# Kernel tuning notes

Measured on AMD Instinct MI355X. Metric: run time of the kernel, lower is better.

Reference implementation:

```python
import jax, jax.numpy as jnp
import numpy as np

N = 50000      # nodes
E = 800000     # edges (before self-loops)
D = 128        # hid_d
H = 8          # heads
C = D // H     # per-head channels
L = 3          # layers
SLOPE = 0.2    # GATv2 leaky_relu negative slope
EPS = 1e-5     # LayerNorm eps


def setup_inputs() -> dict:
    key = jax.random.key(0)
    ks = jax.random.split(key, 8)
    x = jax.random.normal(ks[0], (N, D), dtype=jnp.float32)
    ei = jax.random.randint(ks[1], (2, E), 0, N, dtype=jnp.int32)
    s = 1.0 / np.sqrt(D)
    Wl = jax.random.normal(ks[2], (L, D, D), dtype=jnp.float32) * s   # source transform per layer
    Wr = jax.random.normal(ks[3], (L, D, D), dtype=jnp.float32) * s   # target transform per layer
    att = jax.random.normal(ks[4], (L, H, C), dtype=jnp.float32) * (1.0 / np.sqrt(C))
    bias = jnp.zeros((L, D), dtype=jnp.float32)
    gamma = jnp.ones((L, D), dtype=jnp.float32)
    beta = jnp.zeros((L, D), dtype=jnp.float32)
    return {"x": x, "Wl": Wl, "Wr": Wr, "att": att, "bias": bias,
            "gamma": gamma, "beta": beta, "ei": ei}


def _layernorm(y, g, b):
    mu = jnp.mean(y, axis=-1, keepdims=True)
    var = jnp.mean(jnp.square(y - mu), axis=-1, keepdims=True)
    return (y - mu) * jax.lax.rsqrt(var + EPS) * g + b


def reference(x, Wl, Wr, att, bias, gamma, beta, ei):
    # append self-loops (PyG GATv2Conv default add_self_loops=True)
    loops = jnp.arange(N, dtype=ei.dtype)
    src = jnp.concatenate([ei[0], loops])  # [E+N]
    dst = jnp.concatenate([ei[1], loops])  # [E+N]
    h = x
    for l in range(L):
        xl = (h @ Wl[l]).reshape(N, H, C)   # source-side features
        xr = (h @ Wr[l]).reshape(N, H, C)   # target-side features
        feat = xl[src] + xr[dst]            # [E+N, H, C] per-edge gather
        logits = jnp.einsum('ehc,hc->eh', jax.nn.leaky_relu(feat, SLOPE), att[l])
        # segment softmax over incoming edges of each dst node
        m = jax.ops.segment_max(logits, dst, num_segments=N)
        ex = jnp.exp(logits - m[dst])
        denom = jax.ops.segment_sum(ex, dst, num_segments=N)
        alpha = ex / denom[dst]             # [E+N, H]
        msg = alpha[:, :, None] * xl[src]   # [E+N, H, C]
        out = jax.ops.segment_sum(msg, dst, num_segments=N).reshape(N, H * C) + bias[l]
        # wrapper: h = h + dropout(elu(norm(gat(h)))) ; dropout = identity (eval)
        h = h + jax.nn.elu(_layernorm(out, gamma[l], beta[l]))
    return h
```

## Files before the change

### kernel.cpp

```cpp
#include <hip/hip_runtime.h>
#include <hip/hip_fp16.h>
#include <math.h>

#define N_NODES 50000
#define N_EDGES 800000
#define D 128
#define L 3
#define SLOPE 0.2f
#define LN_EPS 1e-5f
#define ETOT (N_EDGES + N_NODES)
#define SCAN_BLOCKS ((N_NODES + 1023) / 1024)

typedef _Float16 half8 __attribute__((ext_vector_type(8)));
typedef _Float16 h4v  __attribute__((ext_vector_type(4)));
typedef _Float16 h2v  __attribute__((ext_vector_type(2)));
typedef float f32x4 __attribute__((ext_vector_type(4)));


__global__ void rank_hist_kernel(const int* __restrict__ ei, int* __restrict__ counts,
                                 int* __restrict__ rank) {
    int idx = blockIdx.x * blockDim.x + threadIdx.x;
    if (idx >= ETOT) return;
    int d = (idx < N_EDGES) ? ei[N_EDGES + idx] : (idx - N_EDGES);
    rank[idx] = atomicAdd(&counts[d], 1);
}

__global__ __launch_bounds__(1024) void scan1_kernel(const int* __restrict__ counts,
                                                     int* __restrict__ offsets,
                                                     int* __restrict__ bsum,
                                                     int* __restrict__ blockhist) {
    __shared__ int wsum[16];
    __shared__ int lh[256];
    int tid = threadIdx.x;
    if (tid < 256) lh[tid] = 0;
    __syncthreads();
    int lane = tid & 63, w = tid >> 6;
    int i = blockIdx.x * 1024 + tid;
    int v = (i < N_NODES) ? counts[i] : 0;
    if (i < N_NODES) {
        int d = v; if (d > 255) d = 255;
        atomicAdd(&lh[d], 1);
    }
    int sc = v;
    #pragma unroll
    for (int off = 1; off < 64; off <<= 1) {
        int u = __shfl_up(sc, off);
        if (lane >= off) sc += u;
    }
    if (lane == 63) wsum[w] = sc;
    __syncthreads();
    if (w == 0) {
        int t2 = (lane < 16) ? wsum[lane] : 0;
        #pragma unroll
        for (int off = 1; off < 16; off <<= 1) {
            int u = __shfl_up(t2, off);
            if (lane >= off) t2 += u;
        }
        if (lane < 16) wsum[lane] = t2;
    }
    __syncthreads();
    int wpref = (w == 0) ? 0 : wsum[w - 1];
    if (i < N_NODES) offsets[i] = wpref + sc - v;
    if (tid == 0) bsum[blockIdx.x] = wsum[15];
    __syncthreads();
    if (tid < 256) blockhist[blockIdx.x * 256 + tid] = lh[tid];
}

__global__ __launch_bounds__(256) void scan2_kernel(const int* __restrict__ bsum,
                                                    int* __restrict__ bpre,
                                                    int* __restrict__ blockhist) {
    int tid = threadIdx.x;
    if (tid < 64) {
        int lane = tid;
        int v = (lane < SCAN_BLOCKS) ? bsum[lane] : 0;
        int sc = v;
        #pragma unroll
        for (int off = 1; off < 64; off <<= 1) {
            int u = __shfl_up(sc, off);
            if (lane >= off) sc += u;
        }
        if (lane < SCAN_BLOCKS) bpre[lane] = sc - v;
    }
    int d = tid;
    int run = 0;
    #pragma unroll 1
    for (int b = 0; b < SCAN_BLOCKS; ++b) {
        int c = blockhist[b * 256 + d];
        blockhist[b * 256 + d] = run;
        run += c;
    }
    __shared__ int wsum[4];
    int lane = d & 63, w = d >> 6;
    int sc = run;
    #pragma unroll
    for (int off = 1; off < 64; off <<= 1) {
        int u = __shfl_up(sc, off);
        if (lane >= off) sc += u;
    }
    if (lane == 63) wsum[w] = sc;
    __syncthreads();
    int wpre = 0;
    #pragma unroll
    for (int k = 0; k < 4; ++k) wpre += (k < w) ? wsum[k] : 0;
    int binbase = wpre + sc - run;
    #pragma unroll 1
    for (int b = 0; b < SCAN_BLOCKS; ++b)
        blockhist[b * 256 + d] += binbase;
}

__global__ __launch_bounds__(1024) void scan3_kernel(int* __restrict__ offsets,
                                                     const int* __restrict__ bpre,
                                                     const int* __restrict__ counts,
                                                     const int* __restrict__ blockhist,
                                                     int* __restrict__ perm) {
    __shared__ int lh[256];
    int tid = threadIdx.x;
    if (tid < 256) lh[tid] = 0;
    __syncthreads();
    int i = blockIdx.x * 1024 + tid;
    if (i < N_NODES) {
        offsets[i] += bpre[blockIdx.x];
        int d = counts[i]; if (d > 255) d = 255;
        int r = atomicAdd(&lh[d], 1);
        perm[blockhist[blockIdx.x * 256 + d] + r] = i;
    }
    if (i == 0) offsets[N_NODES] = ETOT;
}

__global__ void scatter_kernel(const int* __restrict__ ei, const int* __restrict__ offsets,
                               const int* __restrict__ rank,
                               unsigned short* __restrict__ sorted16) {
    int idx = blockIdx.x * blockDim.x + threadIdx.x;
    if (idx >= ETOT) return;
    int s, d;
    if (idx < N_EDGES) { s = ei[idx]; d = ei[N_EDGES + idx]; }
    else               { s = d = idx - N_EDGES; }
    sorted16[offsets[d] + rank[idx]] = (unsigned short)s;
}


__global__ __launch_bounds__(256) void wfrag_kernel(const float* __restrict__ Wl,
                                                    const float* __restrict__ Wr,
                                                    _Float16* __restrict__ Wfrag) {
    int u = blockIdx.x * 256 + threadIdx.x;
    if (u >= 3 * 4096) return;
    int lane = u & 63, nt = (u >> 6) & 7, kt = (u >> 9) & 3, y = (u >> 11) & 1, l = u >> 12;
    int r = lane & 15, q = lane >> 4;
    const float* W = (y ? Wr : Wl) + (size_t)l * D * D;
    half8 v;
    #pragma unroll
    for (int j = 0; j < 8; ++j)
        v[j] = (_Float16)W[(kt * 32 + q * 8 + j) * D + nt * 16 + r];
    *(half8*)&Wfrag[(size_t)u * 8] = v;
}


template<bool AHALF>
__global__ __launch_bounds__(256) void gemm_mfma_kernel(
        const void* __restrict__ hsrc, const _Float16* __restrict__ WfragL,
        _Float16* __restrict__ xlh, _Float16* __restrict__ xrh) {
    __shared__ half8 Afrag[1024];
    int t = threadIdx.x;
    int row0 = blockIdx.x * 64;
    int w = t >> 6, lane = t & 63;
    int y = w >> 1, nh = w & 1;

    half8 bfrag[16];
    #pragma unroll
    for (int kt = 0; kt < 4; ++kt)
        #pragma unroll
        for (int f = 0; f < 4; ++f) {
            int nt = nh * 4 + f;
            bfrag[kt * 4 + f] =
                *(const half8*)&WfragL[(size_t)(((y * 4 + kt) * 8 + nt) * 64 + lane) * 8];
        }

    {
        int kt = t >> 6, q = (t >> 4) & 3, r = t & 15;
        int kc = kt * 4 + q;
        #pragma unroll
        for (int i = 0; i < 4; ++i) {
            int row = row0 + i * 16 + r;
            half8 v = {};
            if (row < N_NODES) {
                if constexpr (AHALF) {
                    const _Float16* h16 = (const _Float16*)hsrc;
                    v = *(const half8*)&h16[(size_t)row * D + kc * 8];
                } else {
                    const float* p = &((const float*)hsrc)[(size_t)row * D + kc * 8];
                    float4 f0 = *(const float4*)p;
                    float4 f1 = *(const float4*)(p + 4);
                    v[0] = (_Float16)f0.x; v[1] = (_Float16)f0.y;
                    v[2] = (_Float16)f0.z; v[3] = (_Float16)f0.w;
                    v[4] = (_Float16)f1.x; v[5] = (_Float16)f1.y;
                    v[6] = (_Float16)f1.z; v[7] = (_Float16)f1.w;
                }
            }
            Afrag[i * 256 + t] = v;
        }
    }
    __syncthreads();

    f32x4 acc[16];
    #pragma unroll
    for (int i = 0; i < 16; ++i) acc[i] = (f32x4){0.f, 0.f, 0.f, 0.f};
    #pragma unroll
    for (int ntile = 0; ntile < 4; ++ntile) {
        #pragma unroll
        for (int kt = 0; kt < 4; ++kt) {
            half8 a = Afrag[ntile * 256 + kt * 64 + lane];
            #pragma unroll
            for (int f = 0; f < 4; ++f)
                acc[f * 4 + ntile] = __builtin_amdgcn_mfma_f32_16x16x32_f16(
                    bfrag[kt * 4 + f], a, acc[f * 4 + ntile], 0, 0, 0);
        }
    }

    _Float16* out = y ? xrh : xlh;
    int nr = lane & 15, fq = lane >> 4;
    #pragma unroll
    for (int ntile = 0; ntile < 4; ++ntile) {
        int row = row0 + ntile * 16 + nr;
        if (row < N_NODES) {
            #pragma unroll
            for (int f = 0; f < 4; ++f) {
                int fb = nh * 64 + f * 16 + fq * 4;
                h4v v4;
                v4[0] = (_Float16)acc[f * 4 + ntile][0];
                v4[1] = (_Float16)acc[f * 4 + ntile][1];
                v4[2] = (_Float16)acc[f * 4 + ntile][2];
                v4[3] = (_Float16)acc[f * 4 + ntile][3];
                *(h4v*)&out[(size_t)row * D + fb] = v4;
            }
        }
    }
}


__device__ __forceinline__ float pair_reduce2(float p) {
    int t;
    t = __builtin_amdgcn_update_dpp(0, __float_as_int(p), 0xB1, 0xF, 0xF, true);
    p += __int_as_float(t);
    return p;
}

__device__ __forceinline__ float logit8(half8 v, half8 xr, const h2v* att4, h2v slope2) {
    float p = 0.f;
    #pragma unroll
    for (int i = 0; i < 4; ++i) {
        h2v a; a[0] = v[2 * i];  a[1] = v[2 * i + 1];
        h2v b; b[0] = xr[2 * i]; b[1] = xr[2 * i + 1];
        h2v f  = a + b;
        h2v lf = __builtin_elementwise_max(f, f * slope2);
        p = __builtin_amdgcn_fdot2(lf, att4[i], p, false);
    }
    return p;
}

template<int KUN, bool MASK>
__device__ __forceinline__ void edge_block(
        int j, int idx_bp, unsigned off, unsigned laneoff, const char* xlb,
        half8 xr8, const h2v* att4, h2v slope2, int cnt,
        float& s, float* acc) {
    half8 vs[KUN];
    #pragma unroll
    for (int k = 0; k < KUN; ++k) {
        int o = __builtin_amdgcn_ds_bpermute(idx_bp + 4 * (j + k), (int)off);
        vs[k] = *(const half8*)(xlb + ((unsigned)o + laneoff));
    }
    #pragma unroll
    for (int k = 0; k < KUN; ++k) {
        float p = logit8(vs[k], xr8, att4, slope2);
        p = pair_reduce2(p);
        float e = __builtin_amdgcn_exp2f(p);
        if (MASK) e = (j + k < cnt) ? e : 0.f;
        s += e;
        #pragma unroll
        for (int i = 0; i < 8; ++i)
            acc[i] = fmaf(e, (float)vs[k][i], acc[i]);
    }
}

__global__ __launch_bounds__(256) void gat_node_kernel(
        const _Float16* __restrict__ xlh, const _Float16* __restrict__ xrh,
        const int* __restrict__ offsets, const unsigned short* __restrict__ sorted16,
        const int* __restrict__ perm,
        const float* __restrict__ att_l, const float* __restrict__ bias_l,
        const float* __restrict__ gamma_l, const float* __restrict__ beta_l,
        const float* __restrict__ hin, float* __restrict__ hout,
        _Float16* __restrict__ h16out) {
    int wid = (blockIdx.x * blockDim.x + threadIdx.x) >> 6;
    if (wid * 4 >= N_NODES) return;
    int lane = threadIdx.x & 63;
    int g = lane >> 4, hl = lane & 15;
    int node = perm[N_NODES - 4 - wid * 4 + g];
    unsigned laneoff = hl * 16u;
    int idx_bp = g << 6;

    half8 xr8 = *(const half8*)&xrh[(size_t)node * D + hl * 8];
    float4 af0 = *(const float4*)&att_l[hl * 8];
    float4 af1 = *(const float4*)&att_l[hl * 8 + 4];
    h2v att4[4], slope2;
    att4[0][0] = (_Float16)(af0.x * 1.44269504f);
    att4[0][1] = (_Float16)(af0.y * 1.44269504f);
    att4[1][0] = (_Float16)(af0.z * 1.44269504f);
    att4[1][1] = (_Float16)(af0.w * 1.44269504f);
    att4[2][0] = (_Float16)(af1.x * 1.44269504f);
    att4[2][1] = (_Float16)(af1.y * 1.44269504f);
    att4[3][0] = (_Float16)(af1.z * 1.44269504f);
    att4[3][1] = (_Float16)(af1.w * 1.44269504f);
    slope2[0] = (_Float16)SLOPE;
    slope2[1] = (_Float16)SLOPE;

    int beg = offsets[node], end = offsets[node + 1];
    int deg = end - beg;
    int d0 = __builtin_amdgcn_readlane(deg, 0);
    int d1 = __builtin_amdgcn_readlane(deg, 16);
    int d2 = __builtin_amdgcn_readlane(deg, 32);
    int d3 = __builtin_amdgcn_readlane(deg, 48);
    int m01 = d0 > d1 ? d0 : d1, m23 = d2 > d3 ? d2 : d3;
    int degMax = m01 > m23 ? m01 : m23;
    int n01 = d0 < d1 ? d0 : d1, n23 = d2 < d3 ? d2 : d3;
    int degMin = n01 < n23 ? n01 : n23;

    float s = 0.f;
    float acc[8] = {0.f, 0.f, 0.f, 0.f, 0.f, 0.f, 0.f, 0.f};
    const char* xlb = (const char*)xlh;

    for (int c0 = 0; c0 < degMax; c0 += 16) {
        int rem = deg - c0;
        int cnt = rem > 16 ? 16 : rem;
        int cl  = cnt > 0 ? (hl < cnt ? hl : cnt - 1) : 0;
        int pos = cnt > 0 ? beg + c0 + cl : beg;
        unsigned off = ((unsigned)sorted16[pos]) << 8;
        int jmax = degMax - c0; if (jmax > 16) jmax = 16;
        int nfull = degMin - c0; if (nfull > 16) nfull = 16; if (nfull < 0) nfull = 0;
        int j = 0;
        for (; j + 8 <= nfull; j += 8)
            edge_block<8, false>(j, idx_bp, off, laneoff, xlb, xr8, att4, slope2,
                                 cnt, s, acc);
        for (; j + 4 <= nfull; j += 4)
            edge_block<4, false>(j, idx_bp, off, laneoff, xlb, xr8, att4, slope2,
                                 cnt, s, acc);
        for (; j + 4 <= jmax; j += 4)
            edge_block<4, true>(j, idx_bp, off, laneoff, xlb, xr8, att4, slope2,
                                cnt, s, acc);
        for (; j < jmax; ++j)
            edge_block<1, true>(j, idx_bp, off, laneoff, xlb, xr8, att4, slope2,
                                cnt, s, acc);
    }

    float inv = 1.f / s;
    float4 b0 = *(const float4*)&bias_l[hl * 8];
    float4 b1 = *(const float4*)&bias_l[hl * 8 + 4];
    float o[8];
    o[0] = acc[0] * inv + b0.x; o[1] = acc[1] * inv + b0.y;
    o[2] = acc[2] * inv + b0.z; o[3] = acc[3] * inv + b0.w;
    o[4] = acc[4] * inv + b1.x; o[5] = acc[5] * inv + b1.y;
    o[6] = acc[6] * inv + b1.z; o[7] = acc[7] * inv + b1.w;
    float sum = ((o[0] + o[1]) + (o[2] + o[3])) + ((o[4] + o[5]) + (o[6] + o[7]));
    float sq  = ((o[0] * o[0] + o[1] * o[1]) + (o[2] * o[2] + o[3] * o[3]))
              + ((o[4] * o[4] + o[5] * o[5]) + (o[6] * o[6] + o[7] * o[7]));
    #pragma unroll
    for (int msk = 1; msk < 16; msk <<= 1) {
        sum += __shfl_xor(sum, msk);
        sq  += __shfl_xor(sq, msk);
    }
    float mu   = sum * (1.f / 128.f);
    float var  = sq * (1.f / 128.f) - mu * mu;
    float rstd = rsqrtf(var + LN_EPS);
    float4 g0 = *(const float4*)&gamma_l[hl * 8];
    float4 g1 = *(const float4*)&gamma_l[hl * 8 + 4];
    float4 e0 = *(const float4*)&beta_l[hl * 8];
    float4 e1 = *(const float4*)&beta_l[hl * 8 + 4];
    float gam[8] = {g0.x, g0.y, g0.z, g0.w, g1.x, g1.y, g1.z, g1.w};
    float bet[8] = {e0.x, e0.y, e0.z, e0.w, e1.x, e1.y, e1.z, e1.w};
    size_t di = (size_t)node * D + hl * 8;
    float4 h0 = *(const float4*)&hin[di];
    float4 h1 = *(const float4*)&hin[di + 4];
    float hv[8] = {h0.x, h0.y, h0.z, h0.w, h1.x, h1.y, h1.z, h1.w};
    float y[8];
    #pragma unroll
    for (int i = 0; i < 8; ++i) {
        float t = (o[i] - mu) * rstd * gam[i] + bet[i];
        t = t > 0.f ? t : __expf(t) - 1.f;
        y[i] = hv[i] + t;
    }
    float4 w0 = make_float4(y[0], y[1], y[2], y[3]);
    float4 w1 = make_float4(y[4], y[5], y[6], y[7]);
    *(float4*)&hout[di]     = w0;
    *(float4*)&hout[di + 4] = w1;
    half8 h16v;
    #pragma unroll
    for (int i = 0; i < 8; ++i) h16v[i] = (_Float16)y[i];
    *(half8*)&h16out[di] = h16v;
}


extern "C" void kernel_launch(void* const* d_in, const int* in_sizes, int n_in,
                              void* d_out, int out_size, void* d_ws, size_t ws_size,
                              hipStream_t stream) {
    const float* x     = (const float*)d_in[0];
    const float* Wl    = (const float*)d_in[1];
    const float* Wr    = (const float*)d_in[2];
    const float* att   = (const float*)d_in[3];
    const float* bias  = (const float*)d_in[4];
    const float* gamma = (const float*)d_in[5];
    const float* beta  = (const float*)d_in[6];
    const int*   ei    = (const int*)d_in[7];
    float* h = (float*)d_out;

    char* ws = (char*)d_ws;
    _Float16* xlh = (_Float16*)ws;   ws += (size_t)N_NODES * D * sizeof(_Float16);
    _Float16* xrh = (_Float16*)ws;   ws += (size_t)N_NODES * D * sizeof(_Float16);
    _Float16* h16 = (_Float16*)ws;   ws += (size_t)N_NODES * D * sizeof(_Float16);
    _Float16* Wfrag = (_Float16*)ws; ws += (size_t)3 * 4096 * 8 * sizeof(_Float16);
    int* offsets = (int*)ws;         ws += (size_t)(N_NODES + 4) * sizeof(int);
    int* counts  = (int*)ws;         ws += (size_t)N_NODES * sizeof(int);
    int* bsum    = (int*)ws;         ws += 64 * sizeof(int);
    int* bpre    = (int*)ws;         ws += 64 * sizeof(int);
    int* blockhist = (int*)ws;       ws += (size_t)SCAN_BLOCKS * 256 * sizeof(int);
    int* perm    = (int*)ws;         ws += (size_t)N_NODES * sizeof(int);
    int* rank    = (int*)ws;         ws += (size_t)ETOT * sizeof(int);
    unsigned short* sorted16 = (unsigned short*)ws;

    wfrag_kernel<<<48, 256, 0, stream>>>(Wl, Wr, Wfrag);
    (void)hipMemsetAsync(counts, 0, (size_t)N_NODES * sizeof(int), stream);
    rank_hist_kernel<<<(ETOT + 255) / 256, 256, 0, stream>>>(ei, counts, rank);
    scan1_kernel<<<SCAN_BLOCKS, 1024, 0, stream>>>(counts, offsets, bsum, blockhist);
    scan2_kernel<<<1, 256, 0, stream>>>(bsum, bpre, blockhist);
    scan3_kernel<<<SCAN_BLOCKS, 1024, 0, stream>>>(offsets, bpre, counts, blockhist, perm);
    scatter_kernel<<<(ETOT + 255) / 256, 256, 0, stream>>>(ei, offsets, rank, sorted16);

    int gat_waves  = (N_NODES + 3) / 4;
    int gat_blocks = (gat_waves * 64 + 255) / 256;
    for (int l = 0; l < L; ++l) {
        const float* hin = (l == 0) ? x : h;
        if (l == 0)
            gemm_mfma_kernel<false><<<(N_NODES + 63) / 64, 256, 0, stream>>>(
                x, Wfrag + (size_t)l * 4096 * 8, xlh, xrh);
        else
            gemm_mfma_kernel<true><<<(N_NODES + 63) / 64, 256, 0, stream>>>(
                h16, Wfrag + (size_t)l * 4096 * 8, xlh, xrh);
        gat_node_kernel<<<gat_blocks, 256, 0, stream>>>(
            xlh, xrh, offsets, sorted16, perm,
            att + (size_t)l * D, bias + (size_t)l * D,
            gamma + (size_t)l * D, beta + (size_t)l * D, hin, h, h16);
    }
}
```

Baseline: 327.4 us.

## Fuse per-layer GEMM and GAT aggregation into one cooperative persistent kernel

Merges the MFMA projection kernel and the per-node attention/aggregation kernel into a single cooperative kernel per layer. A grid-wide sync separates the two phases, and each phase uses grid-stride loops over tiles and node groups. Grid size comes from an occupancy query that is cached in statics. This removes a kernel launch and its tail per layer, but register pressure from the GEMM phase may reduce occupancy for the latency-bound gather phase.

```diff
diff --git a/kernel.cpp b/kernel.cpp
--- a/kernel.cpp
+++ b/kernel.cpp
@@ -1,6 +1,9 @@
 #include <hip/hip_runtime.h>
+#include <hip/hip_cooperative_groups.h>
 #include <hip/hip_fp16.h>
 #include <math.h>
+
+namespace cg = cooperative_groups;
 
 #define N_NODES 50000
 #define N_EDGES 800000
@@ -155,88 +158,6 @@
 }
 
 
-template<bool AHALF>
-__global__ __launch_bounds__(256) void gemm_mfma_kernel(
-        const void* __restrict__ hsrc, const _Float16* __restrict__ WfragL,
-        _Float16* __restrict__ xlh, _Float16* __restrict__ xrh) {
-    __shared__ half8 Afrag[1024];
-    int t = threadIdx.x;
-    int row0 = blockIdx.x * 64;
-    int w = t >> 6, lane = t & 63;
-    int y = w >> 1, nh = w & 1;
-
-    half8 bfrag[16];
-    #pragma unroll
-    for (int kt = 0; kt < 4; ++kt)
-        #pragma unroll
-        for (int f = 0; f < 4; ++f) {
-            int nt = nh * 4 + f;
-            bfrag[kt * 4 + f] =
-                *(const half8*)&WfragL[(size_t)(((y * 4 + kt) * 8 + nt) * 64 + lane) * 8];
-        }
-
-    {
-        int kt = t >> 6, q = (t >> 4) & 3, r = t & 15;
-        int kc = kt * 4 + q;
-        #pragma unroll
-        for (int i = 0; i < 4; ++i) {
-            int row = row0 + i * 16 + r;
-            half8 v = {};
-            if (row < N_NODES) {
-                if constexpr (AHALF) {
-                    const _Float16* h16 = (const _Float16*)hsrc;
-                    v = *(const half8*)&h16[(size_t)row * D + kc * 8];
-                } else {
-                    const float* p = &((const float*)hsrc)[(size_t)row * D + kc * 8];
-                    float4 f0 = *(const float4*)p;
-                    float4 f1 = *(const float4*)(p + 4);
-                    v[0] = (_Float16)f0.x; v[1] = (_Float16)f0.y;
-                    v[2] = (_Float16)f0.z; v[3] = (_Float16)f0.w;
-                    v[4] = (_Float16)f1.x; v[5] = (_Float16)f1.y;
-                    v[6] = (_Float16)f1.z; v[7] = (_Float16)f1.w;
-                }
-            }
-            Afrag[i * 256 + t] = v;
-        }
-    }
-    __syncthreads();
-
-    f32x4 acc[16];
-    #pragma unroll
-    for (int i = 0; i < 16; ++i) acc[i] = (f32x4){0.f, 0.f, 0.f, 0.f};
-    #pragma unroll
-    for (int ntile = 0; ntile < 4; ++ntile) {
-        #pragma unroll
-        for (int kt = 0; kt < 4; ++kt) {
-            half8 a = Afrag[ntile * 256 + kt * 64 + lane];
-            #pragma unroll
-            for (int f = 0; f < 4; ++f)
-                acc[f * 4 + ntile] = __builtin_amdgcn_mfma_f32_16x16x32_f16(
-                    bfrag[kt * 4 + f], a, acc[f * 4 + ntile], 0, 0, 0);
-        }
-    }
-
-    _Float16* out = y ? xrh : xlh;
-    int nr = lane & 15, fq = lane >> 4;
-    #pragma unroll
-    for (int ntile = 0; ntile < 4; ++ntile) {
-        int row = row0 + ntile * 16 + nr;
-        if (row < N_NODES) {
-            #pragma unroll
-            for (int f = 0; f < 4; ++f) {
-                int fb = nh * 64 + f * 16 + fq * 4;
-                h4v v4;
-                v4[0] = (_Float16)acc[f * 4 + ntile][0];
-                v4[1] = (_Float16)acc[f * 4 + ntile][1];
-                v4[2] = (_Float16)acc[f * 4 + ntile][2];
-                v4[3] = (_Float16)acc[f * 4 + ntile][3];
-                *(h4v*)&out[(size_t)row * D + fb] = v4;
-            }
-        }
-    }
-}
-
-
 __device__ __forceinline__ float pair_reduce2(float p) {
     int t;
     t = __builtin_amdgcn_update_dpp(0, __float_as_int(p), 0xB1, 0xF, 0xF, true);
@@ -281,23 +202,105 @@
     }
 }
 
-__global__ __launch_bounds__(256) void gat_node_kernel(
-        const _Float16* __restrict__ xlh, const _Float16* __restrict__ xrh,
+
+template<bool AHALF>
+__global__ __launch_bounds__(256) void layer_fused_kernel(
+        const void* __restrict__ hsrc, const _Float16* __restrict__ WfragL,
+        _Float16* __restrict__ xlh, _Float16* __restrict__ xrh,
         const int* __restrict__ offsets, const unsigned short* __restrict__ sorted16,
         const int* __restrict__ perm,
         const float* __restrict__ att_l, const float* __restrict__ bias_l,
         const float* __restrict__ gamma_l, const float* __restrict__ beta_l,
         const float* __restrict__ hin, float* __restrict__ hout,
         _Float16* __restrict__ h16out) {
-    int wid = (blockIdx.x * blockDim.x + threadIdx.x) >> 6;
-    if (wid * 4 >= N_NODES) return;
+    __shared__ half8 Afrag[1024];
+    int t = threadIdx.x;
+
+    {
+        int w = t >> 6, lane = t & 63;
+        int y = w >> 1, nh = w & 1;
+        const int NT = (N_NODES + 63) / 64;
+        bool first = true;
+        for (int tile = blockIdx.x; tile < NT; tile += gridDim.x) {
+            int row0 = tile * 64;
+            half8 bfrag[16];
+            #pragma unroll
+            for (int kt = 0; kt < 4; ++kt)
+                #pragma unroll
+                for (int f = 0; f < 4; ++f) {
+                    int nt = nh * 4 + f;
+                    bfrag[kt * 4 + f] =
+                        *(const half8*)&WfragL[(size_t)(((y * 4 + kt) * 8 + nt) * 64 + lane) * 8];
+                }
+            if (!first) __syncthreads();
+            first = false;
+            {
+                int kt = t >> 6, q = (t >> 4) & 3, r = t & 15;
+                int kc = kt * 4 + q;
+                #pragma unroll
+                for (int i = 0; i < 4; ++i) {
+                    int row = row0 + i * 16 + r;
+                    half8 v = {};
+                    if (row < N_NODES) {
+                        if constexpr (AHALF) {
+                            const _Float16* h16 = (const _Float16*)hsrc;
+                            v = *(const half8*)&h16[(size_t)row * D + kc * 8];
+                        } else {
+                            const float* p = &((const float*)hsrc)[(size_t)row * D + kc * 8];
+                            float4 f0 = *(const float4*)p;
+                            float4 f1 = *(const float4*)(p + 4);
+                            v[0] = (_Float16)f0.x; v[1] = (_Float16)f0.y;
+                            v[2] = (_Float16)f0.z; v[3] = (_Float16)f0.w;
+                            v[4] = (_Float16)f1.x; v[5] = (_Float16)f1.y;
+                            v[6] = (_Float16)f1.z; v[7] = (_Float16)f1.w;
+                        }
+                    }
+                    Afrag[i * 256 + t] = v;
+                }
+            }
+            __syncthreads();
+            f32x4 acc[16];
+            #pragma unroll
+            for (int i = 0; i < 16; ++i) acc[i] = (f32x4){0.f, 0.f, 0.f, 0.f};
+            #pragma unroll
+            for (int ntile = 0; ntile < 4; ++ntile) {
+                #pragma unroll
+                for (int kt = 0; kt < 4; ++kt) {
+                    half8 a = Afrag[ntile * 256 + kt * 64 + lane];
+                    #pragma unroll
+                    for (int f = 0; f < 4; ++f)
+                        acc[f * 4 + ntile] = __builtin_amdgcn_mfma_f32_16x16x32_f16(
+                            bfrag[kt * 4 + f], a, acc[f * 4 + ntile], 0, 0, 0);
+                }
+            }
+            _Float16* out = y ? xrh : xlh;
+            int nr = lane & 15, fq = lane >> 4;
+            #pragma unroll
+            for (int ntile = 0; ntile < 4; ++ntile) {
+                int row = row0 + ntile * 16 + nr;
+                if (row < N_NODES) {
+                    #pragma unroll
+                    for (int f = 0; f < 4; ++f) {
+                        int fb = nh * 64 + f * 16 + fq * 4;
+                        h4v v4;
+                        v4[0] = (_Float16)acc[f * 4 + ntile][0];
+                        v4[1] = (_Float16)acc[f * 4 + ntile][1];
+                        v4[2] = (_Float16)acc[f * 4 + ntile][2];
+                        v4[3] = (_Float16)acc[f * 4 + ntile][3];
+                        *(h4v*)&out[(size_t)row * D + fb] = v4;
+                    }
+                }
+            }
+        }
+    }
+
+    cg::this_grid().sync();
+
     int lane = threadIdx.x & 63;
     int g = lane >> 4, hl = lane & 15;
-    int node = perm[N_NODES - 4 - wid * 4 + g];
     unsigned laneoff = hl * 16u;
     int idx_bp = g << 6;
 
-    half8 xr8 = *(const half8*)&xrh[(size_t)node * D + hl * 8];
     float4 af0 = *(const float4*)&att_l[hl * 8];
     float4 af1 = *(const float4*)&att_l[hl * 8 + 4];
     h2v att4[4], slope2;
@@ -311,89 +314,98 @@
     att4[3][1] = (_Float16)(af1.w * 1.44269504f);
     slope2[0] = (_Float16)SLOPE;
     slope2[1] = (_Float16)SLOPE;
-
-    int beg = offsets[node], end = offsets[node + 1];
-    int deg = end - beg;
-    int d0 = __builtin_amdgcn_readlane(deg, 0);
-    int d1 = __builtin_amdgcn_readlane(deg, 16);
-    int d2 = __builtin_amdgcn_readlane(deg, 32);
-    int d3 = __builtin_amdgcn_readlane(deg, 48);
-    int m01 = d0 > d1 ? d0 : d1, m23 = d2 > d3 ? d2 : d3;
-    int degMax = m01 > m23 ? m01 : m23;
-    int n01 = d0 < d1 ? d0 : d1, n23 = d2 < d3 ? d2 : d3;
-    int degMin = n01 < n23 ? n01 : n23;
-
-    float s = 0.f;
-    float acc[8] = {0.f, 0.f, 0.f, 0.f, 0.f, 0.f, 0.f, 0.f};
-    const char* xlb = (const char*)xlh;
-
-    for (int c0 = 0; c0 < degMax; c0 += 16) {
-        int rem = deg - c0;
-        int cnt = rem > 16 ? 16 : rem;
-        int cl  = cnt > 0 ? (hl < cnt ? hl : cnt - 1) : 0;
-        int pos = cnt > 0 ? beg + c0 + cl : beg;
-        unsigned off = ((unsigned)sorted16[pos]) << 8;
-        int jmax = degMax - c0; if (jmax > 16) jmax = 16;
-        int nfull = degMin - c0; if (nfull > 16) nfull = 16; if (nfull < 0) nfull = 0;
-        int j = 0;
-        for (; j + 8 <= nfull; j += 8)
-            edge_block<8, false>(j, idx_bp, off, laneoff, xlb, xr8, att4, slope2,
-                                 cnt, s, acc);
-        for (; j + 4 <= nfull; j += 4)
-            edge_block<4, false>(j, idx_bp, off, laneoff, xlb, xr8, att4, slope2,
-                                 cnt, s, acc);
-        for (; j + 4 <= jmax; j += 4)
-            edge_block<4, true>(j, idx_bp, off, laneoff, xlb, xr8, att4, slope2,
-                                cnt, s, acc);
-        for (; j < jmax; ++j)
-            edge_block<1, true>(j, idx_bp, off, laneoff, xlb, xr8, att4, slope2,
-                                cnt, s, acc);
-    }
-
-    float inv = 1.f / s;
     float4 b0 = *(const float4*)&bias_l[hl * 8];
     float4 b1 = *(const float4*)&bias_l[hl * 8 + 4];
-    float o[8];
-    o[0] = acc[0] * inv + b0.x; o[1] = acc[1] * inv + b0.y;
-    o[2] = acc[2] * inv + b0.z; o[3] = acc[3] * inv + b0.w;
-    o[4] = acc[4] * inv + b1.x; o[5] = acc[5] * inv + b1.y;
-    o[6] = acc[6] * inv + b1.z; o[7] = acc[7] * inv + b1.w;
-    float sum = ((o[0] + o[1]) + (o[2] + o[3])) + ((o[4] + o[5]) + (o[6] + o[7]));
-    float sq  = ((o[0] * o[0] + o[1] * o[1]) + (o[2] * o[2] + o[3] * o[3]))
-              + ((o[4] * o[4] + o[5] * o[5]) + (o[6] * o[6] + o[7] * o[7]));
-    #pragma unroll
-    for (int msk = 1; msk < 16; msk <<= 1) {
-        sum += __shfl_xor(sum, msk);
-        sq  += __shfl_xor(sq, msk);
-    }
-    float mu   = sum * (1.f / 128.f);
-    float var  = sq * (1.f / 128.f) - mu * mu;
-    float rstd = rsqrtf(var + LN_EPS);
-    float4 g0 = *(const float4*)&gamma_l[hl * 8];
-    float4 g1 = *(const float4*)&gamma_l[hl * 8 + 4];
-    float4 e0 = *(const float4*)&beta_l[hl * 8];
-    float4 e1 = *(const float4*)&beta_l[hl * 8 + 4];
-    float gam[8] = {g0.x, g0.y, g0.z, g0.w, g1.x, g1.y, g1.z, g1.w};
-    float bet[8] = {e0.x, e0.y, e0.z, e0.w, e1.x, e1.y, e1.z, e1.w};
-    size_t di = (size_t)node * D + hl * 8;
-    float4 h0 = *(const float4*)&hin[di];
-    float4 h1 = *(const float4*)&hin[di + 4];
-    float hv[8] = {h0.x, h0.y, h0.z, h0.w, h1.x, h1.y, h1.z, h1.w};
-    float y[8];
-    #pragma unroll
-    for (int i = 0; i < 8; ++i) {
-        float t = (o[i] - mu) * rstd * gam[i] + bet[i];
-        t = t > 0.f ? t : __expf(t) - 1.f;
-        y[i] = hv[i] + t;
-    }
-    float4 w0 = make_float4(y[0], y[1], y[2], y[3]);
-    float4 w1 = make_float4(y[4], y[5], y[6], y[7]);
-    *(float4*)&hout[di]     = w0;
-    *(float4*)&hout[di + 4] = w1;
-    half8 h16v;
-    #pragma unroll
-    for (int i = 0; i < 8; ++i) h16v[i] = (_Float16)y[i];
-    *(half8*)&h16out[di] = h16v;
+    float4 gm0 = *(const float4*)&gamma_l[hl * 8];
+    float4 gm1 = *(const float4*)&gamma_l[hl * 8 + 4];
+    float4 bt0 = *(const float4*)&beta_l[hl * 8];
+    float4 bt1 = *(const float4*)&beta_l[hl * 8 + 4];
+    const char* xlb = (const char*)xlh;
+
+    int slot0 = (blockIdx.x * 256 + threadIdx.x) >> 6;
+    int nw = gridDim.x * 4;
+    const int NG = N_NODES / 4;
+
+    for (int slot = slot0; slot < NG; slot += nw) {
+        int node = perm[N_NODES - 4 - slot * 4 + g];
+
+        half8 xr8 = *(const half8*)&xrh[(size_t)node * D + hl * 8];
+        int beg = offsets[node], end = offsets[node + 1];
+        int deg = end - beg;
+        int d0 = __builtin_amdgcn_readlane(deg, 0);
+        int d1 = __builtin_amdgcn_readlane(deg, 16);
+        int d2 = __builtin_amdgcn_readlane(deg, 32);
+        int d3 = __builtin_amdgcn_readlane(deg, 48);
+        int m01 = d0 > d1 ? d0 : d1, m23 = d2 > d3 ? d2 : d3;
+        int degMax = m01 > m23 ? m01 : m23;
+        int n01 = d0 < d1 ? d0 : d1, n23 = d2 < d3 ? d2 : d3;
+        int degMin = n01 < n23 ? n01 : n23;
+
+        float s = 0.f;
+        float acc[8] = {0.f, 0.f, 0.f, 0.f, 0.f, 0.f, 0.f, 0.f};
+
+        for (int c0 = 0; c0 < degMax; c0 += 16) {
+            int rem = deg - c0;
+            int cnt = rem > 16 ? 16 : rem;
+            int cl  = cnt > 0 ? (hl < cnt ? hl : cnt - 1) : 0;
+            int pos = cnt > 0 ? beg + c0 + cl : beg;
+            unsigned off = ((unsigned)sorted16[pos]) << 8;
+            int jmax = degMax - c0; if (jmax > 16) jmax = 16;
+            int nfull = degMin - c0; if (nfull > 16) nfull = 16; if (nfull < 0) nfull = 0;
+            int j = 0;
+            for (; j + 8 <= nfull; j += 8)
+                edge_block<8, false>(j, idx_bp, off, laneoff, xlb, xr8, att4, slope2,
+                                     cnt, s, acc);
+            for (; j + 4 <= nfull; j += 4)
+                edge_block<4, false>(j, idx_bp, off, laneoff, xlb, xr8, att4, slope2,
+                                     cnt, s, acc);
+            for (; j + 4 <= jmax; j += 4)
+                edge_block<4, true>(j, idx_bp, off, laneoff, xlb, xr8, att4, slope2,
+                                    cnt, s, acc);
+            for (; j < jmax; ++j)
+                edge_block<1, true>(j, idx_bp, off, laneoff, xlb, xr8, att4, slope2,
+                                    cnt, s, acc);
+        }
+
+        float inv = 1.f / s;
+        float o[8];
+        o[0] = acc[0] * inv + b0.x; o[1] = acc[1] * inv + b0.y;
+        o[2] = acc[2] * inv + b0.z; o[3] = acc[3] * inv + b0.w;
+        o[4] = acc[4] * inv + b1.x; o[5] = acc[5] * inv + b1.y;
+        o[6] = acc[6] * inv + b1.z; o[7] = acc[7] * inv + b1.w;
+        float sum = ((o[0] + o[1]) + (o[2] + o[3])) + ((o[4] + o[5]) + (o[6] + o[7]));
+        float sq  = ((o[0] * o[0] + o[1] * o[1]) + (o[2] * o[2] + o[3] * o[3]))
+                  + ((o[4] * o[4] + o[5] * o[5]) + (o[6] * o[6] + o[7] * o[7]));
+        #pragma unroll
+        for (int msk = 1; msk < 16; msk <<= 1) {
+            sum += __shfl_xor(sum, msk);
+            sq  += __shfl_xor(sq, msk);
+        }
+        float mu   = sum * (1.f / 128.f);
+        float var  = sq * (1.f / 128.f) - mu * mu;
+        float rstd = rsqrtf(var + LN_EPS);
+        size_t di = (size_t)node * D + hl * 8;
+        float4 h0 = *(const float4*)&hin[di];
+        float4 h1 = *(const float4*)&hin[di + 4];
+        float hv[8] = {h0.x, h0.y, h0.z, h0.w, h1.x, h1.y, h1.z, h1.w};
+        float gam[8] = {gm0.x, gm0.y, gm0.z, gm0.w, gm1.x, gm1.y, gm1.z, gm1.w};
+        float bet[8] = {bt0.x, bt0.y, bt0.z, bt0.w, bt1.x, bt1.y, bt1.z, bt1.w};
+        float yv[8];
+        #pragma unroll
+        for (int i = 0; i < 8; ++i) {
+            float tt = (o[i] - mu) * rstd * gam[i] + bet[i];
+            tt = tt > 0.f ? tt : __expf(tt) - 1.f;
+            yv[i] = hv[i] + tt;
+        }
+        float4 w0 = make_float4(yv[0], yv[1], yv[2], yv[3]);
+        float4 w1 = make_float4(yv[4], yv[5], yv[6], yv[7]);
+        *(float4*)&hout[di]     = w0;
+        *(float4*)&hout[di + 4] = w1;
+        half8 h16v;
+        #pragma unroll
+        for (int i = 0; i < 8; ++i) h16v[i] = (_Float16)yv[i];
+        *(half8*)&h16out[di] = h16v;
+    }
 }
 
 
@@ -424,6 +436,21 @@
     int* rank    = (int*)ws;         ws += (size_t)ETOT * sizeof(int);
     unsigned short* sorted16 = (unsigned short*)ws;
 
+    static int grid_f = 0, grid_t = 0;
+    if (grid_t == 0) {
+        hipDeviceProp_t prop;
+        (void)hipGetDeviceProperties(&prop, 0);
+        int mbF = 0, mbT = 0;
+        (void)hipOccupancyMaxActiveBlocksPerMultiprocessor(
+            &mbF, (const void*)layer_fused_kernel<false>, 256, 0);
+        (void)hipOccupancyMaxActiveBlocksPerMultiprocessor(
+            &mbT, (const void*)layer_fused_kernel<true>, 256, 0);
+        if (mbF < 1) mbF = 1;
+        if (mbT < 1) mbT = 1;
+        grid_f = mbF * prop.multiProcessorCount;
+        grid_t = mbT * prop.multiProcessorCount;
+    }
+
     wfrag_kernel<<<48, 256, 0, stream>>>(Wl, Wr, Wfrag);
     (void)hipMemsetAsync(counts, 0, (size_t)N_NODES * sizeof(int), stream);
     rank_hist_kernel<<<(ETOT + 255) / 256, 256, 0, stream>>>(ei, counts, rank);
@@ -432,19 +459,28 @@
     scan3_kernel<<<SCAN_BLOCKS, 1024, 0, stream>>>(offsets, bpre, counts, blockhist, perm);
     scatter_kernel<<<(ETOT + 255) / 256, 256, 0, stream>>>(ei, offsets, rank, sorted16);
 
-    int gat_waves  = (N_NODES + 3) / 4;
-    int gat_blocks = (gat_waves * 64 + 255) / 256;
     for (int l = 0; l < L; ++l) {
-        const float* hin = (l == 0) ? x : h;
+        const void* hsrc = (l == 0) ? (const void*)x : (const void*)h16;
+        const _Float16* wf = Wfrag + (size_t)l * 4096 * 8;
+        const float* attp   = att + (size_t)l * D;
+        const float* biasp  = bias + (size_t)l * D;
+        const float* gammap = gamma + (size_t)l * D;
+        const float* betap  = beta + (size_t)l * D;
+        const float* hinp   = (l == 0) ? x : h;
+        const int* offp = offsets;
+        const unsigned short* so = sorted16;
+        const int* pp = perm;
+        _Float16* xl_ = xlh; _Float16* xr_ = xrh;
+        float* hp = h; _Float16* h16p = h16;
+        void* args[14] = {&hsrc, &wf, &xl_, &xr_, &offp, &so, &pp,
+                          &attp, &biasp, &gammap, &betap, &hinp, &hp, &h16p};
         if (l == 0)
-            gemm_mfma_kernel<false><<<(N_NODES + 63) / 64, 256, 0, stream>>>(
-                x, Wfrag + (size_t)l * 4096 * 8, xlh, xrh);
+            (void)hipLaunchCooperativeKernel(
+                (const void*)layer_fused_kernel<false>, dim3(grid_f), dim3(256),
+                args, 0, stream);
         else
-            gemm_mfma_kernel<true><<<(N_NODES + 63) / 64, 256, 0, stream>>>(
-                h16, Wfrag + (size_t)l * 4096 * 8, xlh, xrh);
-        gat_node_kernel<<<gat_blocks, 256, 0, stream>>>(
-            xlh, xrh, offsets, sorted16, perm,
-            att + (size_t)l * D, bias + (size_t)l * D,
-            gamma + (size_t)l * D, beta + (size_t)l * D, hin, h, h16);
-    }
-}
+            (void)hipLaunchCooperativeKernel(
+                (const void*)layer_fused_kernel<true>, dim3(grid_t), dim3(256),
+                args, 0, stream);
+    }
+}
```

Result: slower. 534.2 us (+63.1%).
